# Kernel tuning notes

Hardware: AMD Instinct MI355X
Metric: run time of the kernel (lower is better)

## Reference

```python
import jax, jax.numpy as jnp
import numpy as np

N_NODES, N_EDGES, N_GRAPHS = 500000, 8000000, 4096
IN_SIZE, HIDDEN, OUT_SIZE = 11, 16, 4
FEAT = IN_SIZE + 7  # 18; also the (buggy) truncated sequence length in the original


def setup_inputs() -> dict:
    key = jax.random.key(0)
    ks = jax.random.split(key, 10)
    x = jax.random.normal(ks[0], (N_NODES, IN_SIZE), dtype=jnp.float32)
    edge_index = jax.random.randint(ks[1], (2, N_EDGES), 0, N_NODES)
    edge_attr = jax.random.randint(ks[2], (N_EDGES,), 0, 7)
    batch = jnp.sort(jax.random.randint(ks[3], (N_EDGES,), 0, N_GRAPHS))
    s = 0.1
    W_ih = jax.random.normal(ks[4], (4 * HIDDEN, FEAT), jnp.float32) * s
    W_hh = jax.random.normal(ks[5], (4 * HIDDEN, HIDDEN), jnp.float32) * s
    b_ih = jax.random.normal(ks[6], (4 * HIDDEN,), jnp.float32) * s
    b_hh = jax.random.normal(ks[7], (4 * HIDDEN,), jnp.float32) * s
    W_fc = jax.random.normal(ks[8], (OUT_SIZE, HIDDEN), jnp.float32) * s
    b_fc = jax.random.normal(ks[9], (OUT_SIZE,), jnp.float32) * s
    return {"x": x, "W_ih": W_ih, "W_hh": W_hh, "b_ih": b_ih, "b_hh": b_hh,
            "W_fc": W_fc, "b_fc": b_fc, "edge_index": edge_index,
            "edge_attr": edge_attr, "batch": batch, "num_graphs": N_GRAPHS}


def _forward(x, W_ih, W_hh, b_ih, b_hh, W_fc, b_fc, edge_index, edge_attr, batch, num_graphs):
    E = edge_index.shape[1]
    # Per-edge gather: node_value = x[n1] + x[n2], concat one-hot edge type (width 7)
    feat = jnp.concatenate(
        [x[edge_index[0]] + x[edge_index[1]],
         jax.nn.one_hot(edge_attr, 7, dtype=x.dtype)], axis=1)  # [E, FEAT]
    # Position of edge j within its graph: j - index of first edge of that graph
    first = jnp.searchsorted(batch, jnp.arange(num_graphs))  # [B]
    pos = jnp.arange(E) - first[batch]                        # [E], >= 0 (batch sorted)
    # Faithful to original bug: sequences truncated to first FEAT (=18) timesteps.
    # Out-of-range positions dropped by scatter mode='drop'.
    seq = jnp.zeros((num_graphs, FEAT, FEAT), x.dtype).at[batch, pos].set(feat, mode='drop')
    # Single-layer LSTM (torch gate order i, f, g, o), batch_first
    bias = b_ih + b_hh

    def step(carry, xt):
        h, c = carry
        gates = xt @ W_ih.T + h @ W_hh.T + bias  # [B, 4H]
        i, f, g, o = jnp.split(gates, 4, axis=-1)
        c = jax.nn.sigmoid(f) * c + jax.nn.sigmoid(i) * jnp.tanh(g)
        h = jax.nn.sigmoid(o) * jnp.tanh(c)
        return (h, c), None

    h0 = jnp.zeros((num_graphs, HIDDEN), x.dtype)
    (h, c), _ = jax.lax.scan(step, (h0, h0), jnp.swapaxes(seq, 0, 1))  # [T,B,F] scan
    # fc applied then last timestep taken -> equals fc(h_last)
    return h @ W_fc.T + b_fc  # [B, OUT_SIZE]


def reference(x, W_ih, W_hh, b_ih, b_hh, W_fc, b_fc, edge_index, edge_attr, batch, num_graphs):
    return _forward(x, W_ih, W_hh, b_ih, b_hh, W_fc, b_fc, edge_index, edge_attr, batch, num_graphs)
```

## Files before the change

kernel.cpp:

```cpp
#include <hip/hip_runtime.h>

#define IN_SIZE 11
#define HID 16
#define FEAT 18
#define TSTEPS 18

__device__ __forceinline__ float fast_rcp(float v) { return __builtin_amdgcn_rcpf(v); }
__device__ __forceinline__ float fsigmoid(float v) { return fast_rcp(1.0f + __expf(-v)); }
__device__ __forceinline__ float ftanh(float v) {
    v = fminf(fmaxf(v, -15.0f), 15.0f);
    const float e = __expf(2.0f * v);
    return (e - 1.0f) * fast_rcp(e + 1.0f);
}

extern "C" __global__ __launch_bounds__(256, 4)
void tgnn_lstm_fused(const float* __restrict__ x,
                     const float* __restrict__ W_ih,
                     const float* __restrict__ W_hh,
                     const float* __restrict__ b_ih,
                     const float* __restrict__ b_hh,
                     const float* __restrict__ W_fc,
                     const float* __restrict__ b_fc,
                     const int* __restrict__ edge_index,
                     const int* __restrict__ edge_attr,
                     const int* __restrict__ batch,
                     float* __restrict__ out,
                     int E, int B)
{
    __shared__ __align__(16) float feat[4][TSTEPS][20];
    __shared__ __align__(16) float hbuf[4][HID];

    const int wave = threadIdx.x >> 6;
    const int wl   = threadIdx.x & 63;
    const int g    = blockIdx.x * 4 + wave;
    const int u    = wl & 15;
    const int r    = wl >> 4;

    const int row = r * HID + u;
    float wih[FEAT], whh[HID];
#pragma unroll
    for (int k = 0; k < FEAT; ++k) wih[k] = W_ih[row * FEAT + k];
#pragma unroll
    for (int v = 0; v < HID; ++v) whh[v] = W_hh[row * HID + v];
    const float bias = b_ih[row] + b_hh[row];
    const float wfc  = W_fc[row];
    const float bfc  = b_fc[r];

    const int tgt1 = g, tgt2 = g + 1;
    int lo1 = 0, hi1 = E, lo2 = 0, hi2 = E;
    while ((hi1 - lo1) > 64 || (hi2 - lo2) > 64) {
        const unsigned n1 = (unsigned)(hi1 - lo1);
        const unsigned n2 = (unsigned)(hi2 - lo2);
        const int p1 = lo1 + (int)((n1 * (unsigned)wl) >> 6);
        const int p2 = lo2 + (int)((n2 * (unsigned)wl) >> 6);
        const int b1 = batch[p1];
        const int b2 = batch[p2];
        const int c1 = __popcll(__ballot(b1 < tgt1));
        const int c2 = __popcll(__ballot(b2 < tgt2));
        const int nlo1 = c1 ? (lo1 + (int)((n1 * (unsigned)(c1 - 1)) >> 6) + 1) : lo1;
        const int nhi1 = (c1 < 64) ? (lo1 + (int)((n1 * (unsigned)c1) >> 6)) : hi1;
        const int nlo2 = c2 ? (lo2 + (int)((n2 * (unsigned)(c2 - 1)) >> 6) + 1) : lo2;
        const int nhi2 = (c2 < 64) ? (lo2 + (int)((n2 * (unsigned)c2) >> 6)) : hi2;
        lo1 = nlo1; hi1 = nhi1; lo2 = nlo2; hi2 = nhi2;
    }
    {
        const int n1 = hi1 - lo1, n2 = hi2 - lo2;
        int p1 = lo1 + ((wl < n1) ? wl : 0);
        int p2 = lo2 + ((wl < n2) ? wl : 0);
        if (p1 > E - 1) p1 = E - 1;
        if (p2 > E - 1) p2 = E - 1;
        const int b1 = batch[p1];
        const int b2 = batch[p2];
        lo1 += __popcll(__ballot((wl < n1) && (b1 < tgt1)));
        lo2 += __popcll(__ballot((wl < n2) && (b2 < tgt2)));
    }
    const int first = lo1;
    int cnt = lo2 - first;
    cnt = (cnt < 0) ? 0 : ((cnt > TSTEPS) ? TSTEPS : cnt);

    const int side = (wl >= 36) ? 2 : ((wl >= 18) ? 1 : 0);
    const int te   = wl - side * 18;
    int j = first + te;
    if (j > E - 1) j = E - 1;
    int ev = 0;
    if (wl < 54) ev = (side == 2) ? edge_attr[j] : edge_index[side * E + j];

    float* fb = &feat[wave][0][0];
#pragma unroll
    for (int i = 0; i < 4; ++i) {
        const unsigned s  = (unsigned)wl + 64u * (unsigned)i;
        const unsigned t2 = s / 11u;
        const unsigned k2 = s - t2 * 11u;
        const int n1 = __shfl(ev, (int)t2, 64);
        const int n2 = __shfl(ev, (int)t2 + 18, 64);
        const float xa = x[n1 * IN_SIZE + (int)k2];
        const float xb = x[n2 * IN_SIZE + (int)k2];
        if (s < 198u)
            fb[t2 * 20 + k2] = ((int)t2 < cnt) ? (xa + xb) : 0.0f;
    }
#pragma unroll
    for (int i = 0; i < 2; ++i) {
        const unsigned s  = (unsigned)wl + 64u * (unsigned)i;
        const unsigned t2 = s / 7u;
        const unsigned k2 = s - t2 * 7u;
        const int at = __shfl(ev, (int)t2 + 36, 64);
        if (s < 126u)
            fb[t2 * 20 + 11 + k2] = (((int)t2 < cnt) && (at == (int)k2)) ? 1.0f : 0.0f;
    }

    if (r == 0) hbuf[wave][u] = 0.0f;
    float c = 0.0f, h = 0.0f;
    const float4* f4 = reinterpret_cast<const float4*>(fb);
    const float2* f2 = reinterpret_cast<const float2*>(fb);
    const float4* h4 = reinterpret_cast<const float4*>(hbuf[wave]);

    for (int t = 0; t < TSTEPS; ++t) {
        const float4 x0 = f4[t * 5 + 0];
        const float4 x1 = f4[t * 5 + 1];
        const float4 x2 = f4[t * 5 + 2];
        const float4 x3 = f4[t * 5 + 3];
        const float2 x4 = f2[t * 10 + 8];
        const float4 h0 = h4[0], h1 = h4[1], h2 = h4[2], h3 = h4[3];

        float a = bias;
        a = fmaf(x0.x, wih[0],  a); a = fmaf(x0.y, wih[1],  a);
        a = fmaf(x0.z, wih[2],  a); a = fmaf(x0.w, wih[3],  a);
        a = fmaf(x1.x, wih[4],  a); a = fmaf(x1.y, wih[5],  a);
        a = fmaf(x1.z, wih[6],  a); a = fmaf(x1.w, wih[7],  a);
        a = fmaf(x2.x, wih[8],  a); a = fmaf(x2.y, wih[9],  a);
        a = fmaf(x2.z, wih[10], a); a = fmaf(x2.w, wih[11], a);
        a = fmaf(x3.x, wih[12], a); a = fmaf(x3.y, wih[13], a);
        a = fmaf(x3.z, wih[14], a); a = fmaf(x3.w, wih[15], a);
        a = fmaf(x4.x, wih[16], a); a = fmaf(x4.y, wih[17], a);

        a = fmaf(h0.x, whh[0],  a); a = fmaf(h0.y, whh[1],  a);
        a = fmaf(h0.z, whh[2],  a); a = fmaf(h0.w, whh[3],  a);
        a = fmaf(h1.x, whh[4],  a); a = fmaf(h1.y, whh[5],  a);
        a = fmaf(h1.z, whh[6],  a); a = fmaf(h1.w, whh[7],  a);
        a = fmaf(h2.x, whh[8],  a); a = fmaf(h2.y, whh[9],  a);
        a = fmaf(h2.z, whh[10], a); a = fmaf(h2.w, whh[11], a);
        a = fmaf(h3.x, whh[12], a); a = fmaf(h3.y, whh[13], a);
        a = fmaf(h3.z, whh[14], a); a = fmaf(h3.w, whh[15], a);

        const float ai = __shfl(a, u,      64);
        const float af = __shfl(a, u + 16, 64);
        const float ag = __shfl(a, u + 32, 64);
        const float ao = __shfl(a, u + 48, 64);
        const float ig = fsigmoid(ai);
        const float fg = fsigmoid(af);
        const float gg = ftanh(ag);
        const float og = fsigmoid(ao);
        c = fmaf(fg, c, ig * gg);
        h = og * ftanh(c);
        if (r == 0) hbuf[wave][u] = h;
    }

    float p = h * wfc;
#pragma unroll
    for (int m = 8; m >= 1; m >>= 1) p += __shfl_xor(p, m, 16);
    if (u == 0 && g < B) out[g * 4 + r] = p + bfc;
}

extern "C" void kernel_launch(void* const* d_in, const int* in_sizes, int n_in,
                              void* d_out, int out_size, void* d_ws, size_t ws_size,
                              hipStream_t stream) {
    const float* x     = (const float*)d_in[0];
    const float* W_ih  = (const float*)d_in[1];
    const float* W_hh  = (const float*)d_in[2];
    const float* b_ih  = (const float*)d_in[3];
    const float* b_hh  = (const float*)d_in[4];
    const float* W_fc  = (const float*)d_in[5];
    const float* b_fc  = (const float*)d_in[6];
    const int* edge_index = (const int*)d_in[7];
    const int* edge_attr  = (const int*)d_in[8];
    const int* batch      = (const int*)d_in[9];

    const int E = in_sizes[8];
    const int B = out_size / 4;

    const int grid = (B + 3) / 4;
    tgnn_lstm_fused<<<grid, 256, 0, stream>>>(x, W_ih, W_hh, b_ih, b_hh,
                                              W_fc, b_fc,
                                              edge_index, edge_attr, batch,
                                              (float*)d_out, E, B);
}
```

Baseline: 27.86 us.

## Restructure LSTM to precompute input gates and use readlane instead of LDS

Removes the shared-memory feature and hidden-state buffers. Each lane now loads one edge's node features directly, and the one-hot edge-type product is replaced with a single weight-column lookup. All 18 input projections are computed up front, so the recurrent loop only does the 16-wide hidden matvec, with h broadcast via readlane. A single shared sigmoid/tanh formula per lane plus xor shuffles replaces the four per-gate shuffles and separate activations. The trade-off is higher register pressure and many scalar readlane operations per step.

```diff
diff --git a/kernel.cpp b/kernel.cpp
--- a/kernel.cpp
+++ b/kernel.cpp
@@ -6,11 +6,9 @@
 #define TSTEPS 18
 
 __device__ __forceinline__ float fast_rcp(float v) { return __builtin_amdgcn_rcpf(v); }
-__device__ __forceinline__ float fsigmoid(float v) { return fast_rcp(1.0f + __expf(-v)); }
-__device__ __forceinline__ float ftanh(float v) {
-    v = fminf(fmaxf(v, -15.0f), 15.0f);
-    const float e = __expf(2.0f * v);
-    return (e - 1.0f) * fast_rcp(e + 1.0f);
+
+__device__ __forceinline__ float rl(float v, int lane) {
+    return __int_as_float(__builtin_amdgcn_readlane(__float_as_int(v), lane));
 }
 
 extern "C" __global__ __launch_bounds__(256, 4)
@@ -27,19 +25,15 @@
                      float* __restrict__ out,
                      int E, int B)
 {
-    __shared__ __align__(16) float feat[4][TSTEPS][20];
-    __shared__ __align__(16) float hbuf[4][HID];
+    const int wl  = threadIdx.x & 63;
+    const int g   = (blockIdx.x * blockDim.x + threadIdx.x) >> 6;
+    const int u   = wl & 15;
+    const int r   = wl >> 4;
+    const int row = wl;
 
-    const int wave = threadIdx.x >> 6;
-    const int wl   = threadIdx.x & 63;
-    const int g    = blockIdx.x * 4 + wave;
-    const int u    = wl & 15;
-    const int r    = wl >> 4;
-
-    const int row = r * HID + u;
-    float wih[FEAT], whh[HID];
+    float wih[IN_SIZE], whh[HID];
 #pragma unroll
-    for (int k = 0; k < FEAT; ++k) wih[k] = W_ih[row * FEAT + k];
+    for (int k = 0; k < IN_SIZE; ++k) wih[k] = W_ih[row * FEAT + k];
 #pragma unroll
     for (int v = 0; v < HID; ++v) whh[v] = W_hh[row * HID + v];
     const float bias = b_ih[row] + b_hh[row];
@@ -49,113 +43,99 @@
     const int tgt1 = g, tgt2 = g + 1;
     int lo1 = 0, hi1 = E, lo2 = 0, hi2 = E;
     while ((hi1 - lo1) > 64 || (hi2 - lo2) > 64) {
-        const unsigned n1 = (unsigned)(hi1 - lo1);
-        const unsigned n2 = (unsigned)(hi2 - lo2);
-        const int p1 = lo1 + (int)((n1 * (unsigned)wl) >> 6);
-        const int p2 = lo2 + (int)((n2 * (unsigned)wl) >> 6);
+        const unsigned n1r = (unsigned)(hi1 - lo1);
+        const unsigned n2r = (unsigned)(hi2 - lo2);
+        const int p1 = lo1 + (int)((n1r * (unsigned)wl) >> 6);
+        const int p2 = lo2 + (int)((n2r * (unsigned)wl) >> 6);
         const int b1 = batch[p1];
         const int b2 = batch[p2];
         const int c1 = __popcll(__ballot(b1 < tgt1));
         const int c2 = __popcll(__ballot(b2 < tgt2));
-        const int nlo1 = c1 ? (lo1 + (int)((n1 * (unsigned)(c1 - 1)) >> 6) + 1) : lo1;
-        const int nhi1 = (c1 < 64) ? (lo1 + (int)((n1 * (unsigned)c1) >> 6)) : hi1;
-        const int nlo2 = c2 ? (lo2 + (int)((n2 * (unsigned)(c2 - 1)) >> 6) + 1) : lo2;
-        const int nhi2 = (c2 < 64) ? (lo2 + (int)((n2 * (unsigned)c2) >> 6)) : hi2;
+        const int nlo1 = c1 ? (lo1 + (int)((n1r * (unsigned)(c1 - 1)) >> 6) + 1) : lo1;
+        const int nhi1 = (c1 < 64) ? (lo1 + (int)((n1r * (unsigned)c1) >> 6)) : hi1;
+        const int nlo2 = c2 ? (lo2 + (int)((n2r * (unsigned)(c2 - 1)) >> 6) + 1) : lo2;
+        const int nhi2 = (c2 < 64) ? (lo2 + (int)((n2r * (unsigned)c2) >> 6)) : hi2;
         lo1 = nlo1; hi1 = nhi1; lo2 = nlo2; hi2 = nhi2;
     }
     {
-        const int n1 = hi1 - lo1, n2 = hi2 - lo2;
-        int p1 = lo1 + ((wl < n1) ? wl : 0);
-        int p2 = lo2 + ((wl < n2) ? wl : 0);
+        const int n1r = hi1 - lo1, n2r = hi2 - lo2;
+        int p1 = lo1 + ((wl < n1r) ? wl : 0);
+        int p2 = lo2 + ((wl < n2r) ? wl : 0);
         if (p1 > E - 1) p1 = E - 1;
         if (p2 > E - 1) p2 = E - 1;
         const int b1 = batch[p1];
         const int b2 = batch[p2];
-        lo1 += __popcll(__ballot((wl < n1) && (b1 < tgt1)));
-        lo2 += __popcll(__ballot((wl < n2) && (b2 < tgt2)));
+        lo1 += __popcll(__ballot((wl < n1r) && (b1 < tgt1)));
+        lo2 += __popcll(__ballot((wl < n2r) && (b2 < tgt2)));
     }
     const int first = lo1;
     int cnt = lo2 - first;
     cnt = (cnt < 0) ? 0 : ((cnt > TSTEPS) ? TSTEPS : cnt);
 
-    const int side = (wl >= 36) ? 2 : ((wl >= 18) ? 1 : 0);
-    const int te   = wl - side * 18;
-    int j = first + te;
-    if (j > E - 1) j = E - 1;
-    int ev = 0;
-    if (wl < 54) ev = (side == 2) ? edge_attr[j] : edge_index[side * E + j];
-
-    float* fb = &feat[wave][0][0];
+    int n1 = 0, n2 = 0, ea = 0;
+    if (wl < TSTEPS) {
+        int j = first + wl;
+        if (j > E - 1) j = E - 1;
+        n1 = edge_index[j];
+        n2 = edge_index[E + j];
+        ea = edge_attr[j];
+    }
+    float f[IN_SIZE];
+    {
+        const float* xa = x + (long)n1 * IN_SIZE;
+        const float* xb = x + (long)n2 * IN_SIZE;
 #pragma unroll
-    for (int i = 0; i < 4; ++i) {
-        const unsigned s  = (unsigned)wl + 64u * (unsigned)i;
-        const unsigned t2 = s / 11u;
-        const unsigned k2 = s - t2 * 11u;
-        const int n1 = __shfl(ev, (int)t2, 64);
-        const int n2 = __shfl(ev, (int)t2 + 18, 64);
-        const float xa = x[n1 * IN_SIZE + (int)k2];
-        const float xb = x[n2 * IN_SIZE + (int)k2];
-        if (s < 198u)
-            fb[t2 * 20 + k2] = ((int)t2 < cnt) ? (xa + xb) : 0.0f;
+        for (int k = 0; k < IN_SIZE; ++k) f[k] = xa[k] + xb[k];
     }
+    if (wl >= cnt) {
 #pragma unroll
-    for (int i = 0; i < 2; ++i) {
-        const unsigned s  = (unsigned)wl + 64u * (unsigned)i;
-        const unsigned t2 = s / 7u;
-        const unsigned k2 = s - t2 * 7u;
-        const int at = __shfl(ev, (int)t2 + 36, 64);
-        if (s < 126u)
-            fb[t2 * 20 + 11 + k2] = (((int)t2 < cnt) && (at == (int)k2)) ? 1.0f : 0.0f;
+        for (int k = 0; k < IN_SIZE; ++k) f[k] = 0.0f;
     }
 
-    if (r == 0) hbuf[wave][u] = 0.0f;
-    float c = 0.0f, h = 0.0f;
-    const float4* f4 = reinterpret_cast<const float4*>(fb);
-    const float2* f2 = reinterpret_cast<const float2*>(fb);
-    const float4* h4 = reinterpret_cast<const float4*>(hbuf[wave]);
-
+    float ain[TSTEPS];
+#pragma unroll
     for (int t = 0; t < TSTEPS; ++t) {
-        const float4 x0 = f4[t * 5 + 0];
-        const float4 x1 = f4[t * 5 + 1];
-        const float4 x2 = f4[t * 5 + 2];
-        const float4 x3 = f4[t * 5 + 3];
-        const float2 x4 = f2[t * 10 + 8];
-        const float4 h0 = h4[0], h1 = h4[1], h2 = h4[2], h3 = h4[3];
-
-        float a = bias;
-        a = fmaf(x0.x, wih[0],  a); a = fmaf(x0.y, wih[1],  a);
-        a = fmaf(x0.z, wih[2],  a); a = fmaf(x0.w, wih[3],  a);
-        a = fmaf(x1.x, wih[4],  a); a = fmaf(x1.y, wih[5],  a);
-        a = fmaf(x1.z, wih[6],  a); a = fmaf(x1.w, wih[7],  a);
-        a = fmaf(x2.x, wih[8],  a); a = fmaf(x2.y, wih[9],  a);
-        a = fmaf(x2.z, wih[10], a); a = fmaf(x2.w, wih[11], a);
-        a = fmaf(x3.x, wih[12], a); a = fmaf(x3.y, wih[13], a);
-        a = fmaf(x3.z, wih[14], a); a = fmaf(x3.w, wih[15], a);
-        a = fmaf(x4.x, wih[16], a); a = fmaf(x4.y, wih[17], a);
-
-        a = fmaf(h0.x, whh[0],  a); a = fmaf(h0.y, whh[1],  a);
-        a = fmaf(h0.z, whh[2],  a); a = fmaf(h0.w, whh[3],  a);
-        a = fmaf(h1.x, whh[4],  a); a = fmaf(h1.y, whh[5],  a);
-        a = fmaf(h1.z, whh[6],  a); a = fmaf(h1.w, whh[7],  a);
-        a = fmaf(h2.x, whh[8],  a); a = fmaf(h2.y, whh[9],  a);
-        a = fmaf(h2.z, whh[10], a); a = fmaf(h2.w, whh[11], a);
-        a = fmaf(h3.x, whh[12], a); a = fmaf(h3.y, whh[13], a);
-        a = fmaf(h3.z, whh[14], a); a = fmaf(h3.w, whh[15], a);
-
-        const float ai = __shfl(a, u,      64);
-        const float af = __shfl(a, u + 16, 64);
-        const float ag = __shfl(a, u + 32, 64);
-        const float ao = __shfl(a, u + 48, 64);
-        const float ig = fsigmoid(ai);
-        const float fg = fsigmoid(af);
-        const float gg = ftanh(ag);
-        const float og = fsigmoid(ao);
-        c = fmaf(fg, c, ig * gg);
-        h = og * ftanh(c);
-        if (r == 0) hbuf[wave][u] = h;
+        const int eat = __builtin_amdgcn_readlane(ea, t);
+        const float w1 = W_ih[row * FEAT + IN_SIZE + eat];
+        float a = bias + ((t < cnt) ? w1 : 0.0f);
+#pragma unroll
+        for (int k = 0; k < IN_SIZE; ++k)
+            a = fmaf(rl(f[k], t), wih[k], a);
+        ain[t] = a;
     }
 
-    float p = h * wfc;
+    const float sa = (r == 2) ? -2.0f : -1.0f;
+    const float ma = (r == 2) ?  2.0f :  1.0f;
+    const float oa = (r == 2) ? -1.0f :  0.0f;
+
+    float h = 0.0f, c = 0.0f;
+#pragma unroll
+    for (int t = 0; t < TSTEPS; ++t) {
+        float a;
+        if (t == 0) {
+            a = ain[0];
+        } else {
+            float A0 = ain[t], A1 = 0.0f, A2 = 0.0f, A3 = 0.0f;
+#pragma unroll
+            for (int v = 0; v < HID; v += 4) {
+                A0 = fmaf(rl(h, v + 0), whh[v + 0], A0);
+                A1 = fmaf(rl(h, v + 1), whh[v + 1], A1);
+                A2 = fmaf(rl(h, v + 2), whh[v + 2], A2);
+                A3 = fmaf(rl(h, v + 3), whh[v + 3], A3);
+            }
+            a = (A0 + A1) + (A2 + A3);
+        }
+        const float act = fmaf(ma, fast_rcp(1.0f + __expf(sa * a)), oa);
+        const float s1 = __shfl_xor(act, 16, 64);
+        const float s2 = __shfl_xor(act, 32, 64);
+        const float s3 = __shfl_xor(s1, 32, 64);
+        c = fmaf(s1, c, act * s2);
+        const float th = fmaf(2.0f, fast_rcp(1.0f + __expf(-2.0f * c)), -1.0f);
+        h = s3 * th;
+    }
+
+    const float hb = __shfl(h, u, 64);
+    float p = hb * wfc;
 #pragma unroll
     for (int m = 8; m >= 1; m >>= 1) p += __shfl_xor(p, m, 16);
     if (u == 0 && g < B) out[g * 4 + r] = p + bfc;
```

Result: no change. 27.96 us (+0.4%).
